# Kernel optimization log

Measured on AMD Instinct MI355X. Metric: run time of the kernel, lower is better.

The kernel has to match this reference:

```python
import jax, jax.numpy as jnp
import numpy as np
import math

NUM_CONVS = 4
GN_GROUPS = 32
GN_EPS = 1e-5
FPN_STRIDES = (8, 16, 32, 64, 128)
PRIOR_PROB = 0.01


def conv3x3(x, w, b):
    # x: [N,C,H,W], w: [O,I,3,3]
    y = jax.lax.conv_general_dilated(
        x, w, window_strides=(1, 1), padding='SAME',
        dimension_numbers=('NCHW', 'OIHW', 'NCHW'))
    return y + b[None, :, None, None]


def group_norm(x, gamma, beta):
    n, c, h, w = x.shape
    xg = x.reshape(n, GN_GROUPS, c // GN_GROUPS, h, w)
    mean = xg.mean(axis=(2, 3, 4), keepdims=True)
    var = xg.var(axis=(2, 3, 4), keepdims=True)
    xn = ((xg - mean) * jax.lax.rsqrt(var + GN_EPS)).reshape(n, c, h, w)
    return xn * gamma[None, :, None, None] + beta[None, :, None, None]


def subnet(x, ws, bs, gws, gbs):
    # NUM_CONVS x (conv3x3 -> GN -> ReLU)
    for i in range(NUM_CONVS):
        x = jax.nn.relu(group_norm(conv3x3(x, ws[i], bs[i]), gws[i], gbs[i]))
    return x


def permute_to_N_HWA_K(x, k):
    n = x.shape[0]
    return x.transpose(0, 2, 3, 1).reshape(n, -1, k)


def setup_inputs() -> dict:
    key = jax.random.key(0)
    ks = jax.random.split(key, 16)
    C, K = 256, 80
    feats = {
        'p3': jax.random.normal(ks[0], (1, C, 80, 80), jnp.float32),
        'p4': jax.random.normal(ks[1], (1, C, 40, 40), jnp.float32),
        'p5': jax.random.normal(ks[2], (1, C, 20, 20), jnp.float32),
        'p6': jax.random.normal(ks[3], (1, C, 10, 10), jnp.float32),
        'p7': jax.random.normal(ks[4], (1, C, 5, 5), jnp.float32),
    }
    std = 0.01
    bias_value = -math.log((1 - PRIOR_PROB) / PRIOR_PROB)
    params = {
        'cls_w': std * jax.random.normal(ks[5], (NUM_CONVS, C, C, 3, 3), jnp.float32),
        'cls_b': jnp.zeros((NUM_CONVS, C), jnp.float32),
        'cls_gn_w': jnp.ones((NUM_CONVS, C), jnp.float32),
        'cls_gn_b': jnp.zeros((NUM_CONVS, C), jnp.float32),
        'box_w': std * jax.random.normal(ks[6], (NUM_CONVS, C, C, 3, 3), jnp.float32),
        'box_b': jnp.zeros((NUM_CONVS, C), jnp.float32),
        'box_gn_w': jnp.ones((NUM_CONVS, C), jnp.float32),
        'box_gn_b': jnp.zeros((NUM_CONVS, C), jnp.float32),
        'score_w': std * jax.random.normal(ks[7], (K, C, 3, 3), jnp.float32),
        'score_b': jnp.full((K,), bias_value, jnp.float32),
        'pred_w': std * jax.random.normal(ks[8], (4, C, 3, 3), jnp.float32),
        'pred_b': jnp.zeros((4,), jnp.float32),
        'iou_w': std * jax.random.normal(ks[9], (1, C, 3, 3), jnp.float32),
        'iou_b': jnp.zeros((1,), jnp.float32),
        'scales': jnp.ones((5,), jnp.float32),
    }
    return {**feats, **params}


def reference(p3, p4, p5, p6, p7,
              cls_w, cls_b, cls_gn_w, cls_gn_b,
              box_w, box_b, box_gn_w, box_gn_b,
              score_w, score_b, pred_w, pred_b, iou_w, iou_b, scales):
    features = [p3, p4, p5, p6, p7]
    logits, bbox_reg, ious = [], [], []
    for l, feat in enumerate(features):
        c = subnet(feat, cls_w, cls_b, cls_gn_w, cls_gn_b)
        b = subnet(feat, box_w, box_b, box_gn_w, box_gn_b)
        logit = conv3x3(c, score_w, score_b)          # [N,80,H,W]
        iou = conv3x3(b, iou_w, iou_b)                # [N,1,H,W]
        bp = conv3x3(b, pred_w, pred_b) * scales[l]   # Scale module
        # norm_reg_targets=True branch
        reg = jax.nn.relu(bp) * FPN_STRIDES[l]        # [N,4,H,W]
        logits.append(permute_to_N_HWA_K(logit, 80))
        bbox_reg.append(permute_to_N_HWA_K(reg, 4))
        ious.append(permute_to_N_HWA_K(iou, 1))
    box_cls = jnp.concatenate(logits, axis=1)    # [N, sumHW, 80]
    box_delta = jnp.concatenate(bbox_reg, axis=1)  # [N, sumHW, 4]
    box_iou = jnp.concatenate(ious, axis=1)      # [N, sumHW, 1]
    # pack into one array for a single output: [N, sumHW, 85]
    return jnp.concatenate([box_cls, box_delta, box_iou], axis=-1)
```

## Files before the change

kernel.cpp:

```cpp
#include <hip/hip_runtime.h>

typedef unsigned short u16;
typedef __attribute__((ext_vector_type(8))) short bf16x8;
typedef __attribute__((ext_vector_type(4))) float f32x4;

#define NLEV 5
#define CCH 256
#define KTOT 2304
#define P_TOT 8525
#define PP_TOT 9165
#define PLS (PP_TOT*64)
#define HSTR 11776

__constant__ int   c_HW[NLEV]     = {6400, 1600, 400, 100, 25};
__constant__ int   c_W[NLEV]      = {80, 40, 20, 10, 5};
__constant__ int   c_off[NLEV]    = {0, 6400, 8000, 8400, 8500};
__constant__ int   c_poff[NLEV]   = {0, 6724, 8488, 8972, 9116};
__constant__ int   c_tls[NLEV+1]  = {0, 50, 65, 71, 73, 74};
__constant__ int   c_ntx[NLEV]    = {5, 3, 2, 1, 1};
__constant__ float c_stridef[NLEV]= {8.f, 16.f, 32.f, 64.f, 128.f};

__device__ __forceinline__ u16 f2bf(float f){
  union { float f; unsigned u; } v; v.f = f;
  unsigned r = v.u + 0x7fffu + ((v.u >> 16) & 1u);
  return (u16)(r >> 16);
}

__device__ __forceinline__ void g2l16(const u16* g, u16* l, int lane){
#if defined(__has_builtin)
#if __has_builtin(__builtin_amdgcn_global_load_lds)
  __builtin_amdgcn_global_load_lds(
      (const __attribute__((address_space(1))) unsigned int*)g,
      (__attribute__((address_space(3))) unsigned int*)l, 16, 0, 0);
  return;
#endif
#endif
  *(uint4*)(l + lane*8) = *(const uint4*)g;
}

#define WAIT_VM12  0x0F7C

template<int MODE>
__global__ __launch_bounds__(128, 2) void gemm_conv(
    const u16* __restrict__ Xc, const u16* __restrict__ Xb,
    const u16* __restrict__ Wc, const u16* __restrict__ Wb,
    const float* __restrict__ bc, const float* __restrict__ bb,
    float* __restrict__ Yc, float* __restrict__ Yb,
    float* __restrict__ stats,
    const float* __restrict__ predb, const float* __restrict__ ioub,
    const float* __restrict__ scales, float* __restrict__ out)
{
  __shared__ u16 hB[2*HSTR];
  __shared__ float sstat[8][2];

  const int ptile = blockIdx.x;
  const int job   = (MODE == 0) ? 0 : blockIdx.y;
  const int mtile = (MODE == 0) ? blockIdx.y : (job == 1 ? 1 : 0);
  const int br    = (MODE == 0) ? blockIdx.z : (job == 2 ? 1 : 0);
  int lv = 0;
  #pragma unroll
  for (int i = 1; i < NLEV; i++) if (ptile >= c_tls[i]) lv = i;
  const int tidx = ptile - c_tls[lv];
  const int ntx = c_ntx[lv];
  const int ty0 = (tidx / ntx) * 8, tx0 = (tidx - (tidx / ntx) * ntx) * 16;
  const int W = c_W[lv], wrow2 = W + 2;

  const int tid = threadIdx.x, wv = tid >> 6, ln = tid & 63;
  const int quad = ln >> 4, l15 = ln & 15;

  const u16* __restrict__ X  = br ? Xb : Xc;
  const u16* __restrict__ WA = br ? Wb : Wc;

  const int SZ = (MODE == 0) ? 16384 : 8192;
  const int g2 = mtile*2 + wv;
  const u16* aln = WA + (size_t)(g2*2048 + ln*8);

  const u16* hptr[12]; int hslab[12];
  #pragma unroll
  for (int i = 0; i < 12; i++) {
    int j = wv + 2*i;
    if (j > 22) j -= 2;
    hslab[i] = j;
    const int item = j*64 + ln;
    int hp = item >> 3; if (hp >= 180) hp -= 180;
    const int g = item & 7;
    const int hy = hp / 18, hx = hp - hy*18;
    const int prow = c_poff[lv] + (ty0 + hy)*wrow2 + tx0 + hx;
    hptr[i] = X + (size_t)prow*64 + ((g ^ (hp & 7)) << 3);
  }

  auto stageH = [&](int plane) {
    u16* dst = &hB[(plane & 1) * HSTR];
    const size_t cof = (size_t)plane * PLS;
    #pragma unroll
    for (int i = 0; i < 12; i++)
      g2l16(hptr[i] + cof, dst + hslab[i]*512, ln);
  };

  f32x4 acc[2][8];
  #pragma unroll
  for (int i = 0; i < 2; i++)
    #pragma unroll
    for (int j = 0; j < 8; j++) acc[i][j] = (f32x4){0.f, 0.f, 0.f, 0.f};

  bf16x8 afA[3][2][2], afB[3][2][2];
  auto loadA = [&](int cc_, int dw_, bf16x8 (&af)[3][2][2]) {
    #pragma unroll
    for (int dh = 0; dh < 3; dh++) {
      const u16* p = aln + (size_t)((dh*3 + dw_)*4 + cc_) * SZ;
      #pragma unroll
      for (int sub = 0; sub < 2; sub++)
        #pragma unroll
        for (int mt = 0; mt < 2; mt++)
          af[dh][sub][mt] = *(const bf16x8*)(p + (sub*2 + mt)*512);
    }
  };

  if (MODE == 0 && tid < 16) sstat[tid >> 1][tid & 1] = 0.f;

  stageH(0);
  stageH(1);
  loadA(0, 0, afA);
  __syncthreads();

  int cc = 0, dw = 0;
  auto body = [&](int u, bf16x8 (&cur)[3][2][2], bf16x8 (&nxt)[3][2][2]) {
    if (dw == 0 && cc > 0) {
      __builtin_amdgcn_s_waitcnt(WAIT_VM12);
      __builtin_amdgcn_sched_barrier(0);
      __builtin_amdgcn_s_barrier();
      __builtin_amdgcn_sched_barrier(0);
      if (cc < 3) stageH(cc + 1);
    }
    {
      int dwn = dw + 1, ccn = cc;
      if (dwn == 3) { dwn = 0; ccn++; }
      if (u < 11) loadA(ccn, dwn, nxt);
    }
    const u16* hpl = &hB[(cc & 1) * HSTR];
    #pragma unroll
    for (int sub = 0; sub < 2; sub++) {
      const int q = sub*4 + quad;
      bf16x8 bf[10];
      #pragma unroll
      for (int n2 = 0; n2 < 10; n2++) {
        const int hp = n2*18 + l15 + dw;
        bf[n2] = *(const bf16x8*)&hpl[hp*64 + ((q ^ (hp & 7)) << 3)];
      }
      #pragma unroll
      for (int dh = 0; dh < 3; dh++)
        #pragma unroll
        for (int mt = 0; mt < 2; mt++)
          #pragma unroll
          for (int nt = 0; nt < 8; nt++)
            acc[mt][nt] = __builtin_amdgcn_mfma_f32_16x16x32_bf16(
                cur[dh][sub][mt], bf[nt + dh], acc[mt][nt], 0, 0, 0);
    }
    if (++dw == 3) { dw = 0; cc++; }
  };
  #pragma unroll 1
  for (int uu = 0; uu < 12; uu += 2) {
    body(uu,     afA, afB);
    body(uu + 1, afB, afA);
  }

  const int gx = tx0 + l15;
  if (MODE == 0) {
    const float* __restrict__ bias = br ? bb : bc;
    float* __restrict__ Y = br ? Yb : Yc;
    #pragma unroll
    for (int mt = 0; mt < 2; mt++) {
      const int mloc = wv*32 + mt*16 + quad*4;
      const int mrow = mtile*64 + mloc;
      const f32x4 bv = *(const f32x4*)&bias[mrow];
      float s = 0.f, sq = 0.f;
      #pragma unroll
      for (int nt = 0; nt < 8; nt++) {
        const int gy = ty0 + nt;
        f32x4 v = acc[mt][nt] + bv;
        if (gy < W && gx < W) {
          const size_t n = (size_t)(c_off[lv] + gy*W + gx);
          *(f32x4*)&Y[n*CCH + mrow] = v;
          #pragma unroll
          for (int r = 0; r < 4; r++) { s += v[r]; sq += v[r]*v[r]; }
        }
      }
      #pragma unroll
      for (int o = 1; o < 16; o <<= 1) { s += __shfl_xor(s, o); sq += __shfl_xor(sq, o); }
      if (l15 == 0) {
        const int g = mloc >> 3;
        atomicAdd(&sstat[g][0], s);
        atomicAdd(&sstat[g][1], sq);
      }
    }
    __syncthreads();
    if (tid < 16) {
      const int g = tid >> 1, c = tid & 1;
      atomicAdd(&stats[((br*NLEV + lv)*32 + mtile*8 + g)*2 + c], sstat[g][c]);
    }
  } else {
    const float scl = scales[lv];
    const float stf = c_stridef[lv];
    #pragma unroll
    for (int mt = 0; mt < 2; mt++) {
      const int mr0 = mtile*64 + wv*32 + mt*16 + quad*4;
      if (mr0 >= 85) continue;
      #pragma unroll
      for (int nt = 0; nt < 8; nt++) {
        const int gy = ty0 + nt;
        if (gy >= W || gx >= W) continue;
        const size_t n = (size_t)(c_off[lv] + gy*W + gx);
        const f32x4 v = acc[mt][nt];
        #pragma unroll
        for (int r = 0; r < 4; r++) {
          const int m = mr0 + r;
          if (br == 0) {
            if (m < 80) out[n*85 + m] = v[r] + bc[m];
          } else {
            if (m < 4) {
              const float t = (v[r] + predb[m]) * scl;
              out[n*85 + 80 + m] = fmaxf(t, 0.f) * stf;
            } else if (m == 4) {
              out[n*85 + 84] = v[r] + ioub[0];
            }
          }
        }
      }
    }
  }
}

__global__ __launch_bounds__(256) void gn_relu(
    const float* __restrict__ Yc, const float* __restrict__ Yb,
    const float* __restrict__ stats,
    const float* __restrict__ gwc, const float* __restrict__ gbc,
    const float* __restrict__ gwb, const float* __restrict__ gbb,
    u16* __restrict__ Xc, u16* __restrict__ Xb)
{
  const int t = blockIdx.x * 256 + threadIdx.x;
  if (t >= 2 * P_TOT * 32) return;
  const int br = t / (P_TOT * 32);
  const int r  = t - br * (P_TOT * 32);
  const int pg = r >> 5;
  const int c0 = (r & 31) << 3;
  int lv = 0;
  #pragma unroll
  for (int i = 1; i < NLEV; i++) if (pg >= c_off[i]) lv = i;
  const int pl = pg - c_off[lv];
  const int Wl = c_W[lv];
  const int g = c0 >> 3;
  const float* st = &stats[(((size_t)br*NLEV + lv)*32 + g)*2];
  const float cnt = 8.f * (float)c_HW[lv];
  const float mean = st[0] / cnt;
  const float var  = st[1] / cnt - mean*mean;
  const float rstd = rsqrtf(var + 1e-5f);
  const float* Y  = br ? Yb : Yc;
  const float* gw = br ? gwb : gwc;
  const float* gb = br ? gbb : gbc;
  u16* X = br ? Xb : Xc;
  const float* y = &Y[(size_t)pg*CCH + c0];
  const int h = pl / Wl, wi = pl - h*Wl;
  const size_t pidx = (size_t)(c_poff[lv] + (h+1)*(Wl+2) + (wi+1));
  union { u16 u[8]; uint4 v; } pk;
  #pragma unroll
  for (int i = 0; i < 8; i++) {
    const float v = (y[i] - mean)*rstd*gw[c0+i] + gb[c0+i];
    pk.u[i] = f2bf(fmaxf(v, 0.f));
  }
  *(uint4*)&X[(size_t)(c0 >> 6)*PLS + pidx*64 + (c0 & 63)] = pk.v;
}

__global__ __launch_bounds__(256) void feat2bf(
    const float* __restrict__ p3, const float* __restrict__ p4,
    const float* __restrict__ p5, const float* __restrict__ p6,
    const float* __restrict__ p7, u16* __restrict__ X)
{
  const int t = blockIdx.x * 256 + threadIdx.x;
  if (t >= P_TOT * 32) return;
  const int pg = t >> 5, c0 = (t & 31) << 3;
  int lv = 0;
  #pragma unroll
  for (int i = 1; i < NLEV; i++) if (pg >= c_off[i]) lv = i;
  const int pl = pg - c_off[lv];
  const float* src = lv==0 ? p3 : lv==1 ? p4 : lv==2 ? p5 : lv==3 ? p6 : p7;
  const int HW = c_HW[lv], Wl = c_W[lv];
  const int h = pl / Wl, wi = pl - h*Wl;
  const size_t pidx = (size_t)(c_poff[lv] + (h+1)*(Wl+2) + (wi+1));
  union { u16 u[8]; uint4 v; } pk;
  #pragma unroll
  for (int i = 0; i < 8; i++)
    pk.u[i] = f2bf(src[(size_t)(c0+i)*HW + pl]);
  *(uint4*)&X[(size_t)(c0 >> 6)*PLS + pidx*64 + (c0 & 63)] = pk.v;
}

__global__ __launch_bounds__(256) void wconv(
    const float* __restrict__ cw, const float* __restrict__ bw,
    u16* __restrict__ Wc, u16* __restrict__ Wb)
{
  const size_t N = (size_t)4*256*KTOT;
  const size_t t = (size_t)blockIdx.x * 256 + threadIdx.x;
  if (t >= 2*N) return;
  const float* src = (t < N) ? cw : bw;
  u16* dst = (t < N) ? Wc : Wb;
  const size_t i = (t < N) ? t : t - N;
  const size_t lc = i / KTOT;
  const int kk = (int)(i - lc*KTOT);
  const int l = (int)(lc >> 8), co = (int)(lc & 255);
  const int tap = kk >> 8, ci = kk & 255;
  const int s = kk >> 6, kl = kk & 63;
  const size_t d = (size_t)l*589824 + (size_t)s*16384 +
      (size_t)((co >> 5)*2048 + (kl >> 5)*1024 + ((co >> 4) & 1)*512 +
               ((kl >> 3) & 3)*128 + (co & 15)*8 + (kl & 7));
  dst[d] = f2bf(src[(lc*256 + ci)*9 + tap]);
}

__global__ __launch_bounds__(256) void hconv(
    const float* __restrict__ sw, const float* __restrict__ pw,
    const float* __restrict__ iw, u16* __restrict__ Whc, u16* __restrict__ Whb)
{
  const int N = 128 * KTOT;
  const int t = blockIdx.x * 256 + threadIdx.x;
  if (t >= 2*N) return;
  const int i = (t < N) ? t : t - N;
  const int co = i / KTOT, kk = i - co*KTOT;
  const int tap = kk >> 8, ci = kk & 255;
  const int s = kk >> 6, kl = kk & 63;
  const size_t d = (size_t)s*8192 +
      (size_t)((co >> 5)*2048 + (kl >> 5)*1024 + ((co >> 4) & 1)*512 +
               ((kl >> 3) & 3)*128 + (co & 15)*8 + (kl & 7));
  float v = 0.f;
  if (t < N) {
    if (co < 80) v = sw[(co*256 + ci)*9 + tap];
    Whc[d] = f2bf(v);
  } else {
    if (co < 4)       v = pw[(co*256 + ci)*9 + tap];
    else if (co == 4) v = iw[ci*9 + tap];
    Whb[d] = f2bf(v);
  }
}

extern "C" void kernel_launch(void* const* d_in, const int* in_sizes, int n_in,
                              void* d_out, int out_size, void* d_ws, size_t ws_size,
                              hipStream_t stream)
{
  const float* p3      = (const float*)d_in[0];
  const float* p4      = (const float*)d_in[1];
  const float* p5      = (const float*)d_in[2];
  const float* p6      = (const float*)d_in[3];
  const float* p7      = (const float*)d_in[4];
  const float* cls_w   = (const float*)d_in[5];
  const float* cls_b   = (const float*)d_in[6];
  const float* cls_gw  = (const float*)d_in[7];
  const float* cls_gb  = (const float*)d_in[8];
  const float* box_w   = (const float*)d_in[9];
  const float* box_b   = (const float*)d_in[10];
  const float* box_gw  = (const float*)d_in[11];
  const float* box_gb  = (const float*)d_in[12];
  const float* score_w = (const float*)d_in[13];
  const float* score_b = (const float*)d_in[14];
  const float* pred_w  = (const float*)d_in[15];
  const float* pred_b  = (const float*)d_in[16];
  const float* iou_w   = (const float*)d_in[17];
  const float* iou_b   = (const float*)d_in[18];
  const float* scales  = (const float*)d_in[19];
  float* out = (float*)d_out;

  char* w = (char*)d_ws;
  size_t o = 0;
  auto alloc = [&](size_t b) { void* p = w + o; o += (b + 255) & ~(size_t)255; return p; };
  u16*   XF = (u16*)alloc((size_t)PP_TOT*CCH*2);
  u16*   XC = (u16*)alloc((size_t)PP_TOT*CCH*2);
  u16*   XB = (u16*)alloc((size_t)PP_TOT*CCH*2);
  float* ST = (float*)alloc((size_t)4*2*NLEV*32*2*4);
  u16*  WRC = (u16*)alloc((size_t)4*256*KTOT*2);
  u16*  WRB = (u16*)alloc((size_t)4*256*KTOT*2);
  u16*  WHC = (u16*)alloc((size_t)128*KTOT*2);
  u16*  WHB = (u16*)alloc((size_t)128*KTOT*2);
  float* YC = (float*)alloc((size_t)P_TOT*CCH*4);
  float* YB = (float*)alloc((size_t)P_TOT*CCH*4);

  hipMemsetAsync(XF, 0, (size_t)3*PP_TOT*CCH*2 + (size_t)4*2*NLEV*32*2*4, stream);

  wconv<<<dim3((unsigned)(((size_t)2*4*256*KTOT + 255)/256)), 256, 0, stream>>>(cls_w, box_w, WRC, WRB);
  hconv<<<dim3((2*128*KTOT + 255)/256), 256, 0, stream>>>(score_w, pred_w, iou_w, WHC, WHB);
  feat2bf<<<dim3((P_TOT*32 + 255)/256), 256, 0, stream>>>(p3, p4, p5, p6, p7, XF);

  const u16* xci = XF; const u16* xbi = XF;
  for (int l = 0; l < 4; l++) {
    float* STl = ST + (size_t)l*2*NLEV*32*2;
    gemm_conv<0><<<dim3(74, 4, 2), 128, 0, stream>>>(
        xci, xbi, WRC + (size_t)l*589824, WRB + (size_t)l*589824,
        cls_b + l*256, box_b + l*256, YC, YB, STl,
        nullptr, nullptr, nullptr, nullptr);
    gn_relu<<<dim3((2*P_TOT*32 + 255)/256), 256, 0, stream>>>(
        YC, YB, STl, cls_gw + l*256, cls_gb + l*256, box_gw + l*256, box_gb + l*256,
        XC, XB);
    xci = XC; xbi = XB;
  }
  gemm_conv<1><<<dim3(74, 3, 1), 128, 0, stream>>>(
      xci, xbi, WHC, WHB, score_b, nullptr, nullptr, nullptr, nullptr,
      pred_b, iou_b, scales, out);
}
```

Baseline: 328.9 us.

## Split conv GEMM tile across four waves with single-buffered LDS halo

Moves the implicit-GEMM conv block from 2 to 4 waves, so each wave owns one 16-row M subtile instead of two, halving accumulator and A-fragment registers. The LDS halo goes from double-buffered to single-buffered, with a load-then-wait-then-barrier per channel plane. GN statistics are now atomically added straight to global memory, dropping the shared reduction. Fewer registers and less LDS per block are meant to raise occupancy and hide latency. The cost is that halo loads no longer overlap compute, there is an extra barrier per plane, and global atomics increase.

```diff
diff --git a/kernel.cpp b/kernel.cpp
--- a/kernel.cpp
+++ b/kernel.cpp
@@ -38,10 +38,10 @@
   *(uint4*)(l + lane*8) = *(const uint4*)g;
 }
 
-#define WAIT_VM12  0x0F7C
+#define WAIT_VM0   0x0F70
 
 template<int MODE>
-__global__ __launch_bounds__(128, 2) void gemm_conv(
+__global__ __launch_bounds__(256, 3) void gemm_conv(
     const u16* __restrict__ Xc, const u16* __restrict__ Xb,
     const u16* __restrict__ Wc, const u16* __restrict__ Wb,
     const float* __restrict__ bc, const float* __restrict__ bb,
@@ -50,8 +50,7 @@
     const float* __restrict__ predb, const float* __restrict__ ioub,
     const float* __restrict__ scales, float* __restrict__ out)
 {
-  __shared__ u16 hB[2*HSTR];
-  __shared__ float sstat[8][2];
+  __shared__ u16 hB[HSTR];
 
   const int ptile = blockIdx.x;
   const int job   = (MODE == 0) ? 0 : blockIdx.y;
@@ -67,77 +66,68 @@
 
   const int tid = threadIdx.x, wv = tid >> 6, ln = tid & 63;
   const int quad = ln >> 4, l15 = ln & 15;
+  const int mtSel = wv & 1;
+  const int g2 = mtile*2 + (wv >> 1);
 
   const u16* __restrict__ X  = br ? Xb : Xc;
   const u16* __restrict__ WA = br ? Wb : Wc;
 
   const int SZ = (MODE == 0) ? 16384 : 8192;
-  const int g2 = mtile*2 + wv;
   const u16* aln = WA + (size_t)(g2*2048 + ln*8);
 
-  const u16* hptr[12]; int hslab[12];
-  #pragma unroll
-  for (int i = 0; i < 12; i++) {
-    int j = wv + 2*i;
-    if (j > 22) j -= 2;
-    hslab[i] = j;
-    const int item = j*64 + ln;
-    int hp = item >> 3; if (hp >= 180) hp -= 180;
-    const int g = item & 7;
-    const int hy = hp / 18, hx = hp - hy*18;
-    const int prow = c_poff[lv] + (ty0 + hy)*wrow2 + tx0 + hx;
-    hptr[i] = X + (size_t)prow*64 + ((g ^ (hp & 7)) << 3);
-  }
-
   auto stageH = [&](int plane) {
-    u16* dst = &hB[(plane & 1) * HSTR];
     const size_t cof = (size_t)plane * PLS;
     #pragma unroll
-    for (int i = 0; i < 12; i++)
-      g2l16(hptr[i] + cof, dst + hslab[i]*512, ln);
+    for (int i = 0; i < 6; i++) {
+      int jj = wv + 4*i;
+      if (jj > 22) jj -= 4;
+      const int item = jj*64 + ln;
+      int hp = item >> 3; if (hp >= 180) hp -= 180;
+      const int g = item & 7;
+      const int hy = hp / 18, hx = hp - hy*18;
+      const int prow = c_poff[lv] + (ty0 + hy)*wrow2 + tx0 + hx;
+      g2l16(X + (size_t)prow*64 + ((g ^ (hp & 7)) << 3) + cof,
+            hB + jj*512, ln);
+    }
   };
 
-  f32x4 acc[2][8];
-  #pragma unroll
-  for (int i = 0; i < 2; i++)
-    #pragma unroll
-    for (int j = 0; j < 8; j++) acc[i][j] = (f32x4){0.f, 0.f, 0.f, 0.f};
-
-  bf16x8 afA[3][2][2], afB[3][2][2];
-  auto loadA = [&](int cc_, int dw_, bf16x8 (&af)[3][2][2]) {
+  f32x4 acc[8];
+  #pragma unroll
+  for (int jj = 0; jj < 8; jj++) acc[jj] = (f32x4){0.f, 0.f, 0.f, 0.f};
+
+  bf16x8 afA[3][2], afB[3][2];
+  auto loadA = [&](int cc_, int dw_, bf16x8 (&af)[3][2]) {
     #pragma unroll
     for (int dh = 0; dh < 3; dh++) {
       const u16* p = aln + (size_t)((dh*3 + dw_)*4 + cc_) * SZ;
       #pragma unroll
       for (int sub = 0; sub < 2; sub++)
-        #pragma unroll
-        for (int mt = 0; mt < 2; mt++)
-          af[dh][sub][mt] = *(const bf16x8*)(p + (sub*2 + mt)*512);
+        af[dh][sub] = *(const bf16x8*)(p + (sub*2 + mtSel)*512);
     }
   };
 
-  if (MODE == 0 && tid < 16) sstat[tid >> 1][tid & 1] = 0.f;
-
   stageH(0);
-  stageH(1);
   loadA(0, 0, afA);
+  __builtin_amdgcn_s_waitcnt(WAIT_VM0);
   __syncthreads();
 
   int cc = 0, dw = 0;
-  auto body = [&](int u, bf16x8 (&cur)[3][2][2], bf16x8 (&nxt)[3][2][2]) {
+  auto body = [&](int u, bf16x8 (&cur)[3][2], bf16x8 (&nxt)[3][2]) {
     if (dw == 0 && cc > 0) {
-      __builtin_amdgcn_s_waitcnt(WAIT_VM12);
       __builtin_amdgcn_sched_barrier(0);
       __builtin_amdgcn_s_barrier();
       __builtin_amdgcn_sched_barrier(0);
-      if (cc < 3) stageH(cc + 1);
+      stageH(cc);
+      __builtin_amdgcn_s_waitcnt(WAIT_VM0);
+      __builtin_amdgcn_sched_barrier(0);
+      __builtin_amdgcn_s_barrier();
+      __builtin_amdgcn_sched_barrier(0);
     }
     {
       int dwn = dw + 1, ccn = cc;
       if (dwn == 3) { dwn = 0; ccn++; }
       if (u < 11) loadA(ccn, dwn, nxt);
     }
-    const u16* hpl = &hB[(cc & 1) * HSTR];
     #pragma unroll
     for (int sub = 0; sub < 2; sub++) {
       const int q = sub*4 + quad;
@@ -145,16 +135,14 @@
       #pragma unroll
       for (int n2 = 0; n2 < 10; n2++) {
         const int hp = n2*18 + l15 + dw;
-        bf[n2] = *(const bf16x8*)&hpl[hp*64 + ((q ^ (hp & 7)) << 3)];
+        bf[n2] = *(const bf16x8*)&hB[hp*64 + ((q ^ (hp & 7)) << 3)];
       }
       #pragma unroll
       for (int dh = 0; dh < 3; dh++)
         #pragma unroll
-        for (int mt = 0; mt < 2; mt++)
-          #pragma unroll
-          for (int nt = 0; nt < 8; nt++)
-            acc[mt][nt] = __builtin_amdgcn_mfma_f32_16x16x32_bf16(
-                cur[dh][sub][mt], bf[nt + dh], acc[mt][nt], 0, 0, 0);
+        for (int nt = 0; nt < 8; nt++)
+          acc[nt] = __builtin_amdgcn_mfma_f32_16x16x32_bf16(
+              cur[dh][sub], bf[nt + dh], acc[nt], 0, 0, 0);
     }
     if (++dw == 3) { dw = 0; cc++; }
   };
@@ -168,49 +156,38 @@
   if (MODE == 0) {
     const float* __restrict__ bias = br ? bb : bc;
     float* __restrict__ Y = br ? Yb : Yc;
-    #pragma unroll
-    for (int mt = 0; mt < 2; mt++) {
-      const int mloc = wv*32 + mt*16 + quad*4;
-      const int mrow = mtile*64 + mloc;
-      const f32x4 bv = *(const f32x4*)&bias[mrow];
-      float s = 0.f, sq = 0.f;
-      #pragma unroll
-      for (int nt = 0; nt < 8; nt++) {
-        const int gy = ty0 + nt;
-        f32x4 v = acc[mt][nt] + bv;
-        if (gy < W && gx < W) {
-          const size_t n = (size_t)(c_off[lv] + gy*W + gx);
-          *(f32x4*)&Y[n*CCH + mrow] = v;
-          #pragma unroll
-          for (int r = 0; r < 4; r++) { s += v[r]; sq += v[r]*v[r]; }
-        }
+    const int mrow = mtile*64 + wv*16 + quad*4;
+    const f32x4 bv = *(const f32x4*)&bias[mrow];
+    float s = 0.f, sq = 0.f;
+    #pragma unroll
+    for (int nt = 0; nt < 8; nt++) {
+      const int gy = ty0 + nt;
+      f32x4 v = acc[nt] + bv;
+      if (gy < W && gx < W) {
+        const size_t n = (size_t)(c_off[lv] + gy*W + gx);
+        *(f32x4*)&Y[n*CCH + mrow] = v;
+        #pragma unroll
+        for (int r = 0; r < 4; r++) { s += v[r]; sq += v[r]*v[r]; }
       }
-      #pragma unroll
-      for (int o = 1; o < 16; o <<= 1) { s += __shfl_xor(s, o); sq += __shfl_xor(sq, o); }
-      if (l15 == 0) {
-        const int g = mloc >> 3;
-        atomicAdd(&sstat[g][0], s);
-        atomicAdd(&sstat[g][1], sq);
-      }
-    }
-    __syncthreads();
-    if (tid < 16) {
-      const int g = tid >> 1, c = tid & 1;
-      atomicAdd(&stats[((br*NLEV + lv)*32 + mtile*8 + g)*2 + c], sstat[g][c]);
+    }
+    #pragma unroll
+    for (int o = 1; o < 16; o <<= 1) { s += __shfl_xor(s, o); sq += __shfl_xor(sq, o); }
+    if (l15 == 0) {
+      const int G = mrow >> 3;
+      atomicAdd(&stats[((br*NLEV + lv)*32 + G)*2 + 0], s);
+      atomicAdd(&stats[((br*NLEV + lv)*32 + G)*2 + 1], sq);
     }
   } else {
     const float scl = scales[lv];
     const float stf = c_stridef[lv];
-    #pragma unroll
-    for (int mt = 0; mt < 2; mt++) {
-      const int mr0 = mtile*64 + wv*32 + mt*16 + quad*4;
-      if (mr0 >= 85) continue;
+    const int mr0 = mtile*64 + wv*16 + quad*4;
+    if (mr0 < 85) {
       #pragma unroll
       for (int nt = 0; nt < 8; nt++) {
         const int gy = ty0 + nt;
         if (gy >= W || gx >= W) continue;
         const size_t n = (size_t)(c_off[lv] + gy*W + gx);
-        const f32x4 v = acc[mt][nt];
+        const f32x4 v = acc[nt];
         #pragma unroll
         for (int r = 0; r < 4; r++) {
           const int m = mr0 + r;
@@ -388,7 +365,7 @@
   const u16* xci = XF; const u16* xbi = XF;
   for (int l = 0; l < 4; l++) {
     float* STl = ST + (size_t)l*2*NLEV*32*2;
-    gemm_conv<0><<<dim3(74, 4, 2), 128, 0, stream>>>(
+    gemm_conv<0><<<dim3(74, 4, 2), 256, 0, stream>>>(
         xci, xbi, WRC + (size_t)l*589824, WRB + (size_t)l*589824,
         cls_b + l*256, box_b + l*256, YC, YB, STl,
         nullptr, nullptr, nullptr, nullptr);
@@ -397,7 +374,7 @@
         XC, XB);
     xci = XC; xbi = XB;
   }
-  gemm_conv<1><<<dim3(74, 3, 1), 128, 0, stream>>>(
+  gemm_conv<1><<<dim3(74, 3, 1), 256, 0, stream>>>(
       xci, xbi, WHC, WHB, score_b, nullptr, nullptr, nullptr, nullptr,
       pred_b, iou_b, scales, out);
 }
```

Measured after the change: 422.8 us. 1.29x slower.

## Single-buffer halo LDS tile to raise occupancy to three blocks per CU

Applied to the files above, without the earlier changes.

Replaces the double-buffered activation halo in LDS with a single buffer and loads each channel plane synchronously between two barriers. Address arithmetic is recomputed inline instead of keeping 12 precomputed pointers in registers, and the LDS reduction of GN statistics is replaced by direct global atomics. Launch bounds go from 2 to 3 blocks per CU, aiming for more occupancy and fewer registers. In exchange the overlap between halo loads and MFMA compute is lost, and global atomic traffic on the stats increases.

```diff
diff --git a/kernel.cpp b/kernel.cpp
--- a/kernel.cpp
+++ b/kernel.cpp
@@ -38,10 +38,10 @@
   *(uint4*)(l + lane*8) = *(const uint4*)g;
 }
 
-#define WAIT_VM12  0x0F7C
+#define WAIT_VM0   0x0F70
 
 template<int MODE>
-__global__ __launch_bounds__(128, 2) void gemm_conv(
+__global__ __launch_bounds__(128, 3) void gemm_conv(
     const u16* __restrict__ Xc, const u16* __restrict__ Xb,
     const u16* __restrict__ Wc, const u16* __restrict__ Wb,
     const float* __restrict__ bc, const float* __restrict__ bb,
@@ -50,8 +50,7 @@
     const float* __restrict__ predb, const float* __restrict__ ioub,
     const float* __restrict__ scales, float* __restrict__ out)
 {
-  __shared__ u16 hB[2*HSTR];
-  __shared__ float sstat[8][2];
+  __shared__ u16 hB[HSTR];
 
   const int ptile = blockIdx.x;
   const int job   = (MODE == 0) ? 0 : blockIdx.y;
@@ -75,33 +74,27 @@
   const int g2 = mtile*2 + wv;
   const u16* aln = WA + (size_t)(g2*2048 + ln*8);
 
-  const u16* hptr[12]; int hslab[12];
-  #pragma unroll
-  for (int i = 0; i < 12; i++) {
-    int j = wv + 2*i;
-    if (j > 22) j -= 2;
-    hslab[i] = j;
-    const int item = j*64 + ln;
-    int hp = item >> 3; if (hp >= 180) hp -= 180;
-    const int g = item & 7;
-    const int hy = hp / 18, hx = hp - hy*18;
-    const int prow = c_poff[lv] + (ty0 + hy)*wrow2 + tx0 + hx;
-    hptr[i] = X + (size_t)prow*64 + ((g ^ (hp & 7)) << 3);
-  }
-
   auto stageH = [&](int plane) {
-    u16* dst = &hB[(plane & 1) * HSTR];
     const size_t cof = (size_t)plane * PLS;
     #pragma unroll
-    for (int i = 0; i < 12; i++)
-      g2l16(hptr[i] + cof, dst + hslab[i]*512, ln);
+    for (int i = 0; i < 12; i++) {
+      int jj = wv + 2*i;
+      if (jj > 22) jj -= 2;
+      const int item = jj*64 + ln;
+      int hp = item >> 3; if (hp >= 180) hp -= 180;
+      const int g = item & 7;
+      const int hy = hp / 18, hx = hp - hy*18;
+      const int prow = c_poff[lv] + (ty0 + hy)*wrow2 + tx0 + hx;
+      g2l16(X + (size_t)prow*64 + ((g ^ (hp & 7)) << 3) + cof,
+            hB + jj*512, ln);
+    }
   };
 
   f32x4 acc[2][8];
   #pragma unroll
   for (int i = 0; i < 2; i++)
     #pragma unroll
-    for (int j = 0; j < 8; j++) acc[i][j] = (f32x4){0.f, 0.f, 0.f, 0.f};
+    for (int jj = 0; jj < 8; jj++) acc[i][jj] = (f32x4){0.f, 0.f, 0.f, 0.f};
 
   bf16x8 afA[3][2][2], afB[3][2][2];
   auto loadA = [&](int cc_, int dw_, bf16x8 (&af)[3][2][2]) {
@@ -116,28 +109,28 @@
     }
   };
 
-  if (MODE == 0 && tid < 16) sstat[tid >> 1][tid & 1] = 0.f;
-
   stageH(0);
-  stageH(1);
   loadA(0, 0, afA);
+  __builtin_amdgcn_s_waitcnt(WAIT_VM0);
   __syncthreads();
 
   int cc = 0, dw = 0;
   auto body = [&](int u, bf16x8 (&cur)[3][2][2], bf16x8 (&nxt)[3][2][2]) {
     if (dw == 0 && cc > 0) {
-      __builtin_amdgcn_s_waitcnt(WAIT_VM12);
       __builtin_amdgcn_sched_barrier(0);
       __builtin_amdgcn_s_barrier();
       __builtin_amdgcn_sched_barrier(0);
-      if (cc < 3) stageH(cc + 1);
+      stageH(cc);
+      __builtin_amdgcn_s_waitcnt(WAIT_VM0);
+      __builtin_amdgcn_sched_barrier(0);
+      __builtin_amdgcn_s_barrier();
+      __builtin_amdgcn_sched_barrier(0);
     }
     {
       int dwn = dw + 1, ccn = cc;
       if (dwn == 3) { dwn = 0; ccn++; }
       if (u < 11) loadA(ccn, dwn, nxt);
     }
-    const u16* hpl = &hB[(cc & 1) * HSTR];
     #pragma unroll
     for (int sub = 0; sub < 2; sub++) {
       const int q = sub*4 + quad;
@@ -145,7 +138,7 @@
       #pragma unroll
       for (int n2 = 0; n2 < 10; n2++) {
         const int hp = n2*18 + l15 + dw;
-        bf[n2] = *(const bf16x8*)&hpl[hp*64 + ((q ^ (hp & 7)) << 3)];
+        bf[n2] = *(const bf16x8*)&hB[hp*64 + ((q ^ (hp & 7)) << 3)];
       }
       #pragma unroll
       for (int dh = 0; dh < 3; dh++)
@@ -170,8 +163,7 @@
     float* __restrict__ Y = br ? Yb : Yc;
     #pragma unroll
     for (int mt = 0; mt < 2; mt++) {
-      const int mloc = wv*32 + mt*16 + quad*4;
-      const int mrow = mtile*64 + mloc;
+      const int mrow = mtile*64 + wv*32 + mt*16 + quad*4;
       const f32x4 bv = *(const f32x4*)&bias[mrow];
       float s = 0.f, sq = 0.f;
       #pragma unroll
@@ -188,15 +180,10 @@
       #pragma unroll
       for (int o = 1; o < 16; o <<= 1) { s += __shfl_xor(s, o); sq += __shfl_xor(sq, o); }
       if (l15 == 0) {
-        const int g = mloc >> 3;
-        atomicAdd(&sstat[g][0], s);
-        atomicAdd(&sstat[g][1], sq);
+        const int G = mrow >> 3;
+        atomicAdd(&stats[((br*NLEV + lv)*32 + G)*2 + 0], s);
+        atomicAdd(&stats[((br*NLEV + lv)*32 + G)*2 + 1], sq);
       }
-    }
-    __syncthreads();
-    if (tid < 16) {
-      const int g = tid >> 1, c = tid & 1;
-      atomicAdd(&stats[((br*NLEV + lv)*32 + mtile*8 + g)*2 + c], sstat[g][c]);
     }
   } else {
     const float scl = scales[lv];
```

New measurement: 600.0 us. +82.4%, slower.
